# Kernel tuning notes

Hardware: AMD Instinct MI355X
Metric: run time of the kernel (lower is better)

Reference implementation:

```python
import jax, jax.numpy as jnp
import numpy as np

B, T, U = 8, 200, 100
E, P, H, V = 512, 640, 512, 1024


def setup_inputs() -> dict:
    key = jax.random.key(0)
    ks = jax.random.split(key, 8)
    def xavier(k, fan_in, fan_out, gain=0.1):
        bound = gain * np.sqrt(6.0 / (fan_in + fan_out))
        return jax.random.uniform(k, (fan_out, fan_in), jnp.float32, -bound, bound)
    return {
        "encoder_outputs": jax.random.normal(ks[0], (B, T, E), jnp.float32),
        "predictor_outputs": jax.random.normal(ks[1], (B, U, P), jnp.float32),
        "W_enc": xavier(ks[2], E, H),
        "b_enc": jnp.zeros((H,), jnp.float32),
        "W_pred": xavier(ks[3], P, H),
        "b_pred": jnp.zeros((H,), jnp.float32),
        "W_out": xavier(ks[4], H, V),
        "b_out": jnp.zeros((V,), jnp.float32),
    }


def reference(encoder_outputs, predictor_outputs, W_enc, b_enc, W_pred, b_pred, W_out, b_out):
    # project: (B,T,H) and (B,U,H)
    enc = jnp.einsum('bte,he->bth', encoder_outputs, W_enc) + b_enc
    pred = jnp.einsum('bup,hp->buh', predictor_outputs, W_pred) + b_pred
    # broadcast add -> (B,T,U,H), relu (dropout is identity at eval)
    joint = jax.nn.relu(enc[:, :, None, :] + pred[:, None, :, :])
    # output projection -> (B,T,U,V), scaled by 0.1
    out = jnp.einsum('btuh,vh->btuv', joint, W_out) + b_out
    return out * 0.1
```

## Files before the change

### kernel.cpp

```cpp
#include <hip/hip_runtime.h>
#include <hip/hip_bf16.h>
#include <cstdint>
#include <cstddef>

typedef __attribute__((ext_vector_type(8))) __bf16 bf16x8;
typedef __attribute__((ext_vector_type(4))) __bf16 bf16x4;
typedef __attribute__((ext_vector_type(4))) float  f32x4;

#define B_  8
#define T_  200
#define U_  100
#define E_  512
#define P_  640
#define H_  512
#define V_  1024

__device__ __forceinline__ void async_ld16(const void* g, void* lds) {
  __builtin_amdgcn_global_load_lds(
      (const __attribute__((address_space(1))) unsigned int*)g,
      (__attribute__((address_space(3))) unsigned int*)lds,
      16, 0, 0);
}

__global__ void cvt_bf16_kernel(const float* __restrict__ in, __bf16* __restrict__ out, int n) {
  int i = (blockIdx.x * blockDim.x + threadIdx.x) * 4;
  if (i + 4 <= n) {
    f32x4 v = *(const f32x4*)(in + i);
    bf16x4 o;
    o[0] = (__bf16)v[0]; o[1] = (__bf16)v[1]; o[2] = (__bf16)v[2]; o[3] = (__bf16)v[3];
    *(bf16x4*)(out + i) = o;
  } else {
    for (; i < n; ++i) out[i] = (__bf16)in[i];
  }
}

__global__ __launch_bounds__(256)
void gemm_bias_kernel(const __bf16* __restrict__ A, const __bf16* __restrict__ Bm,
                      const float* __restrict__ bias, float* __restrict__ C,
                      int M, int K, int ldc) {
  __shared__ __bf16 As[128 * 32];
  __shared__ __bf16 Bs[128 * 32];

  const int tid  = threadIdx.x;
  const int wave = tid >> 6, lane = tid & 63;
  const int l15  = lane & 15, quad = lane >> 4;
  const int wm   = wave & 1,  wn   = wave >> 1;
  const int m0 = blockIdx.y * 128, n0 = blockIdx.x * 128;

  f32x4 acc[4][4];
#pragma unroll
  for (int i = 0; i < 4; ++i)
#pragma unroll
    for (int j = 0; j < 4; ++j) acc[i][j] = (f32x4){0.f, 0.f, 0.f, 0.f};

  for (int kk = 0; kk < K; kk += 32) {
#pragma unroll
    for (int j = 0; j < 2; ++j) {
      int f   = (wave * 2 + j) * 1024 + lane * 16;
      int row = f >> 6;
      int kb  = (f & 63) >> 1;
      int ar  = m0 + row; if (ar >= M) ar = M - 1;
      async_ld16(A  + (size_t)ar * K + kk + kb,        (char*)As + (wave * 2 + j) * 1024);
      async_ld16(Bm + (size_t)(n0 + row) * K + kk + kb,(char*)Bs + (wave * 2 + j) * 1024);
    }
    __syncthreads();
    bf16x8 af[4], bfr[4];
#pragma unroll
    for (int mi = 0; mi < 4; ++mi)
      af[mi] = *(const bf16x8*)(As + (wm * 64 + mi * 16 + l15) * 32 + quad * 8);
#pragma unroll
    for (int ni = 0; ni < 4; ++ni)
      bfr[ni] = *(const bf16x8*)(Bs + (wn * 64 + ni * 16 + l15) * 32 + quad * 8);
#pragma unroll
    for (int mi = 0; mi < 4; ++mi)
#pragma unroll
      for (int ni = 0; ni < 4; ++ni)
        acc[mi][ni] = __builtin_amdgcn_mfma_f32_16x16x32_bf16(af[mi], bfr[ni], acc[mi][ni], 0, 0, 0);
    __syncthreads();
  }

#pragma unroll
  for (int ni = 0; ni < 4; ++ni) {
    int n = n0 + wn * 64 + ni * 16 + l15;
    float bo = bias[n];
#pragma unroll
    for (int mi = 0; mi < 4; ++mi) {
      int mb = m0 + wm * 64 + mi * 16 + quad * 4;
#pragma unroll
      for (int r = 0; r < 4; ++r) {
        int m = mb + r;
        if (m < M) C[(size_t)m * ldc + n] = acc[mi][ni][r] + bo;
      }
    }
  }
}

__global__ __launch_bounds__(256)
void fused_joint_kernel(const float* __restrict__ enc, const float* __restrict__ pred,
                        const __bf16* __restrict__ Wout, const float* __restrict__ b_out,
                        float* __restrict__ out) {
  __shared__ __bf16 As[128 * 40];
  __shared__ __bf16 Bs[128 * 32];

  const int tid  = threadIdx.x;
  const int wave = tid >> 6, lane = tid & 63;
  const int l15  = lane & 15, quad = lane >> 4;
  const int wm   = wave & 1,  wn   = wave >> 1;
  const int n0 = blockIdx.x * 128;
  const int m0 = blockIdx.y * 128;

  const int r   = tid >> 1;
  const int kof = (tid & 1) << 4;
  const int m   = m0 + r;
  const int u   = m % U_;
  const int bt  = m / U_;
  const int b   = bt / T_;
  const float* encp  = enc  + (size_t)bt * H_ + kof;
  const float* predp = pred + ((size_t)b * U_ + u) * H_ + kof;
  __bf16* asp = As + r * 40 + kof;

  f32x4 acc[4][4];
#pragma unroll
  for (int i = 0; i < 4; ++i)
#pragma unroll
    for (int j = 0; j < 4; ++j) acc[i][j] = (f32x4){0.f, 0.f, 0.f, 0.f};

  for (int kk = 0; kk < H_; kk += 32) {
#pragma unroll
    for (int j = 0; j < 2; ++j) {
      int f   = (wave * 2 + j) * 1024 + lane * 16;
      int row = f >> 6;
      int kb  = (f & 63) >> 1;
      async_ld16(Wout + (size_t)(n0 + row) * H_ + kk + kb, (char*)Bs + (wave * 2 + j) * 1024);
    }
    f32x4 ef[4], pf[4];
#pragma unroll
    for (int i = 0; i < 4; ++i) {
      ef[i] = *(const f32x4*)(encp  + kk + i * 4);
      pf[i] = *(const f32x4*)(predp + kk + i * 4);
    }
    bf16x8 q0, q1;
#pragma unroll
    for (int i = 0; i < 8; ++i) {
      float v0 = fmaxf(ef[i >> 2][i & 3] + pf[i >> 2][i & 3], 0.f);
      float v1 = fmaxf(ef[(i + 8) >> 2][(i + 8) & 3] + pf[(i + 8) >> 2][(i + 8) & 3], 0.f);
      q0[i] = (__bf16)v0;
      q1[i] = (__bf16)v1;
    }
    *(bf16x8*)asp       = q0;
    *((bf16x8*)asp + 1) = q1;
    __syncthreads();

    bf16x8 af[4], bfr[4];
#pragma unroll
    for (int mi = 0; mi < 4; ++mi)
      af[mi] = *(const bf16x8*)(As + (wm * 64 + mi * 16 + l15) * 40 + quad * 8);
#pragma unroll
    for (int ni = 0; ni < 4; ++ni)
      bfr[ni] = *(const bf16x8*)(Bs + (wn * 64 + ni * 16 + l15) * 32 + quad * 8);
#pragma unroll
    for (int mi = 0; mi < 4; ++mi)
#pragma unroll
      for (int ni = 0; ni < 4; ++ni)
        acc[mi][ni] = __builtin_amdgcn_mfma_f32_16x16x32_bf16(af[mi], bfr[ni], acc[mi][ni], 0, 0, 0);
    __syncthreads();
  }

#pragma unroll
  for (int ni = 0; ni < 4; ++ni) {
    int n = n0 + wn * 64 + ni * 16 + l15;
    float bo = b_out[n];
#pragma unroll
    for (int mi = 0; mi < 4; ++mi) {
      size_t mb = (size_t)m0 + wm * 64 + mi * 16 + quad * 4;
      float* op = out + mb * V_ + n;
#pragma unroll
      for (int rr = 0; rr < 4; ++rr)
        op[(size_t)rr * V_] = (acc[mi][ni][rr] + bo) * 0.1f;
    }
  }
}

extern "C" void kernel_launch(void* const* d_in, const int* in_sizes, int n_in,
                              void* d_out, int out_size, void* d_ws, size_t ws_size,
                              hipStream_t stream) {
  const float* encoder   = (const float*)d_in[0];
  const float* predictor = (const float*)d_in[1];
  const float* W_enc     = (const float*)d_in[2];
  const float* b_enc     = (const float*)d_in[3];
  const float* W_pred    = (const float*)d_in[4];
  const float* b_pred    = (const float*)d_in[5];
  const float* W_out     = (const float*)d_in[6];
  const float* b_out     = (const float*)d_in[7];
  float* out = (float*)d_out;

  char* ws = (char*)d_ws;
  size_t off = 0;
  auto alloc = [&](size_t bytes) { char* p = ws + off; off += (bytes + 255) & ~(size_t)255; return p; };

  float*  enc_f    = (float*)alloc((size_t)1600 * 512 * 4);
  float*  pred_f   = (float*)alloc((size_t)800 * 512 * 4);
  __bf16* enc_bf   = (__bf16*)alloc((size_t)1600 * 512 * 2);
  __bf16* Wenc_bf  = (__bf16*)alloc((size_t)512 * 512 * 2);
  __bf16* pred_bf  = (__bf16*)alloc((size_t)800 * 640 * 2);
  __bf16* Wpred_bf = (__bf16*)alloc((size_t)512 * 640 * 2);
  __bf16* Wout_bf  = (__bf16*)alloc((size_t)1024 * 512 * 2);

  auto cvt = [&](const float* src, __bf16* dst, int n) {
    cvt_bf16_kernel<<<(n + 1023) / 1024, 256, 0, stream>>>(src, dst, n);
  };
  cvt(encoder,   enc_bf,   1600 * 512);
  cvt(W_enc,     Wenc_bf,  512 * 512);
  cvt(predictor, pred_bf,  800 * 640);
  cvt(W_pred,    Wpred_bf, 512 * 640);
  cvt(W_out,     Wout_bf,  1024 * 512);

  gemm_bias_kernel<<<dim3(4, 13), 256, 0, stream>>>(enc_bf, Wenc_bf, b_enc, enc_f, 1600, 512, 512);
  gemm_bias_kernel<<<dim3(4, 7), 256, 0, stream>>>(pred_bf, Wpred_bf, b_pred, pred_f, 800, 640, 512);

  fused_joint_kernel<<<dim3(8, 1250), 256, 0, stream>>>(enc_f, pred_f, Wout_bf, b_out, out);
}
```

Before: 963.6 us.

## Materialize bf16 joint tensor and run generic GEMM; merge conversion launches

When the workspace is large enough, a separate kernel builds the relu(enc+pred) joint tensor once in bf16. The output projection then runs through the async-LDS GEMM kernel, which now takes a scale argument. This removes the eightfold recomputation of the joint activations and the synchronous fp32 loads inside the fused kernel's main loop. The cost is writing and re-reading about 164 MB of intermediate data. The five bf16 conversion launches are also merged into one kernel, and the old fused kernel stays as a fallback when the workspace is too small.

After: 1.115 ms. 1.16x slower.

```diff
diff --git a/kernel.cpp b/kernel.cpp
--- a/kernel.cpp
+++ b/kernel.cpp
@@ -22,22 +22,51 @@
       16, 0, 0);
 }
 
-__global__ void cvt_bf16_kernel(const float* __restrict__ in, __bf16* __restrict__ out, int n) {
-  int i = (blockIdx.x * blockDim.x + threadIdx.x) * 4;
-  if (i + 4 <= n) {
-    f32x4 v = *(const f32x4*)(in + i);
-    bf16x4 o;
-    o[0] = (__bf16)v[0]; o[1] = (__bf16)v[1]; o[2] = (__bf16)v[2]; o[3] = (__bf16)v[3];
-    *(bf16x4*)(out + i) = o;
-  } else {
-    for (; i < n; ++i) out[i] = (__bf16)in[i];
-  }
+__global__ __launch_bounds__(256)
+void cvt_all_kernel(const float* s0, __bf16* d0, const float* s1, __bf16* d1,
+                    const float* s2, __bf16* d2, const float* s3, __bf16* d3,
+                    const float* s4, __bf16* d4,
+                    int e0, int e1, int e2, int e3) {
+  int blk = blockIdx.x;
+  const float* s; __bf16* d; int base;
+  if      (blk < e0) { s = s0; d = d0; base = blk; }
+  else if (blk < e1) { s = s1; d = d1; base = blk - e0; }
+  else if (blk < e2) { s = s2; d = d2; base = blk - e1; }
+  else if (blk < e3) { s = s3; d = d3; base = blk - e2; }
+  else               { s = s4; d = d4; base = blk - e3; }
+  int i = base * 1024 + threadIdx.x * 4;
+  f32x4 v = *(const f32x4*)(s + i);
+  bf16x4 o;
+  o[0] = (__bf16)v[0]; o[1] = (__bf16)v[1]; o[2] = (__bf16)v[2]; o[3] = (__bf16)v[3];
+  *(bf16x4*)(d + i) = o;
+}
+
+__global__ __launch_bounds__(256)
+void build_joint_kernel(const float* __restrict__ enc, const float* __restrict__ pred,
+                        __bf16* __restrict__ out) {
+  int m    = blockIdx.x * 4 + (threadIdx.x >> 6);
+  int lane = threadIdx.x & 63;
+  int h0   = lane * 8;
+  int bt = m / U_;
+  int u  = m - bt * U_;
+  int b  = bt / T_;
+  const float* ep = enc  + (size_t)bt * H_ + h0;
+  const float* pp = pred + ((size_t)b * U_ + u) * H_ + h0;
+  f32x4 e0 = *(const f32x4*)ep, e1 = *(const f32x4*)(ep + 4);
+  f32x4 p0 = *(const f32x4*)pp, p1 = *(const f32x4*)(pp + 4);
+  bf16x8 q;
+#pragma unroll
+  for (int i = 0; i < 4; ++i) {
+    q[i]     = (__bf16)fmaxf(e0[i] + p0[i], 0.f);
+    q[i + 4] = (__bf16)fmaxf(e1[i] + p1[i], 0.f);
+  }
+  *(bf16x8*)(out + (size_t)m * H_ + h0) = q;
 }
 
 __global__ __launch_bounds__(256)
 void gemm_bias_kernel(const __bf16* __restrict__ A, const __bf16* __restrict__ Bm,
                       const float* __restrict__ bias, float* __restrict__ C,
-                      int M, int K, int ldc) {
+                      int M, int K, int ldc, float scale) {
   __shared__ __bf16 As[128 * 32];
   __shared__ __bf16 Bs[128 * 32];
 
@@ -89,7 +118,7 @@
 #pragma unroll
       for (int r = 0; r < 4; ++r) {
         int m = mb + r;
-        if (m < M) C[(size_t)m * ldc + n] = acc[mi][ni][r] + bo;
+        if (m < M) C[(size_t)m * ldc + n] = (acc[mi][ni][r] + bo) * scale;
       }
     }
   }
@@ -205,18 +234,21 @@
   __bf16* pred_bf  = (__bf16*)alloc((size_t)800 * 640 * 2);
   __bf16* Wpred_bf = (__bf16*)alloc((size_t)512 * 640 * 2);
   __bf16* Wout_bf  = (__bf16*)alloc((size_t)1024 * 512 * 2);
-
-  auto cvt = [&](const float* src, __bf16* dst, int n) {
-    cvt_bf16_kernel<<<(n + 1023) / 1024, 256, 0, stream>>>(src, dst, n);
-  };
-  cvt(encoder,   enc_bf,   1600 * 512);
-  cvt(W_enc,     Wenc_bf,  512 * 512);
-  cvt(predictor, pred_bf,  800 * 640);
-  cvt(W_pred,    Wpred_bf, 512 * 640);
-  cvt(W_out,     Wout_bf,  1024 * 512);
-
-  gemm_bias_kernel<<<dim3(4, 13), 256, 0, stream>>>(enc_bf, Wenc_bf, b_enc, enc_f, 1600, 512, 512);
-  gemm_bias_kernel<<<dim3(4, 7), 256, 0, stream>>>(pred_bf, Wpred_bf, b_pred, pred_f, 800, 640, 512);
-
-  fused_joint_kernel<<<dim3(8, 1250), 256, 0, stream>>>(enc_f, pred_f, Wout_bf, b_out, out);
-}
+  __bf16* joint_bf = (__bf16*)alloc((size_t)160000 * 512 * 2);
+  bool big_ws = (off <= ws_size);
+
+  cvt_all_kernel<<<2388, 256, 0, stream>>>(
+      encoder, enc_bf, W_enc, Wenc_bf, predictor, pred_bf, W_pred, Wpred_bf,
+      W_out, Wout_bf, 800, 1056, 1556, 1876);
+
+  gemm_bias_kernel<<<dim3(4, 13), 256, 0, stream>>>(enc_bf, Wenc_bf, b_enc, enc_f, 1600, 512, 512, 1.0f);
+  gemm_bias_kernel<<<dim3(4, 7), 256, 0, stream>>>(pred_bf, Wpred_bf, b_pred, pred_f, 800, 640, 512, 1.0f);
+
+  if (big_ws) {
+    build_joint_kernel<<<160000 / 4, 256, 0, stream>>>(enc_f, pred_f, joint_bf);
+    gemm_bias_kernel<<<dim3(8, 1250), 256, 0, stream>>>(joint_bf, Wout_bf, b_out, out,
+                                                        160000, 512, 1024, 0.1f);
+  } else {
+    fused_joint_kernel<<<dim3(8, 1250), 256, 0, stream>>>(enc_f, pred_f, Wout_bf, b_out, out);
+  }
+}
```
